# Optimization experiments

Hardware: AMD Instinct MI355X
Metric: run time of the kernel (lower is better)

## Reference

```python
import jax, jax.numpy as jnp
import numpy as np

B, IN, V, H, OUT = 4096, 1024, 48, 512, 64

def setup_inputs() -> dict:
    key = jax.random.key(0)
    ks = jax.random.split(key, 6)
    s = 0.02
    x = jax.random.normal(ks[0], (B, IN), dtype=jnp.float32)
    # stacked per-vocab MLP params: hidden layers have bias, last layer bias=False
    W1 = jax.random.normal(ks[1], (V, IN, H), dtype=jnp.float32) * s
    b1 = jax.random.normal(ks[2], (V, H), dtype=jnp.float32) * s
    W2 = jax.random.normal(ks[3], (V, H, H), dtype=jnp.float32) * s
    b2 = jax.random.normal(ks[4], (V, H), dtype=jnp.float32) * s
    W3 = jax.random.normal(ks[5], (V, H, OUT), dtype=jnp.float32) * s
    return {"x": x, "W1": W1, "b1": b1, "W2": W2, "b2": b2, "W3": W3}

def reference(x, W1, b1, W2, b2, W3):
    # grouped GEMM over the vocab axis; equivalent to the per-MLP loop + cat
    h = jax.nn.relu(jnp.einsum('bi,vih->bvh', x, W1) + b1)      # [B, V, H]
    h = jax.nn.relu(jnp.einsum('bvh,vhk->bvk', h, W2) + b2)     # [B, V, H]
    o = jnp.einsum('bvk,vko->bvo', h, W3)                        # [B, V, OUT]
    # torch.cat([...], dim=-1) == reshape since outputs are in vocab order
    return o.reshape(x.shape[0], V * OUT)
```

## Files before the change

kernel.cpp:

```cpp
#include <hip/hip_runtime.h>

#define B_SZ   4096
#define IN_SZ  1024
#define V_SZ   48
#define H_SZ   512
#define OUT_SZ 64

typedef __attribute__((ext_vector_type(4))) float f32x4;
typedef __attribute__((ext_vector_type(8))) short bf16x8;
typedef __attribute__((ext_vector_type(4))) short short4v;
typedef __attribute__((ext_vector_type(4))) float float4v;

__device__ __forceinline__ short f2bf(float f){
    unsigned u = __builtin_bit_cast(unsigned, f);
    u += 0x7fffu + ((u >> 16) & 1u);
    return (short)(u >> 16);
}

__device__ __forceinline__ void gl2lds16(const void* g, void* l){
    __builtin_amdgcn_global_load_lds(
        (const __attribute__((address_space(1))) void*)g,
        (__attribute__((address_space(3))) void*)l, 16, 0, 0);
}

__global__ void k_convert_x(const float* __restrict__ x, short* __restrict__ xb){
    int i = blockIdx.x * 256 + threadIdx.x;
    float4v f = ((const float4v*)x)[i];
    short4v o = { f2bf(f.x), f2bf(f.y), f2bf(f.z), f2bf(f.w) };
    ((short4v*)xb)[i] = o;
}

__global__ void k_transpose_cvt(const float* __restrict__ in, short* __restrict__ out,
                                int R, int C){
    __shared__ short t[64][66];
    int v  = blockIdx.z;
    int c0 = blockIdx.x * 64, r0 = blockIdx.y * 64;
    int tx = threadIdx.x, ty = threadIdx.y;
    size_t base = (size_t)v * R * C;
    const float* inp = in + base + (size_t)r0 * C + c0;
    #pragma unroll
    for (int j = 0; j < 16; ++j){
        int r = ty + j*4;
        t[r][tx] = f2bf(inp[(size_t)r * C + tx]);
    }
    __syncthreads();
    short* outp = out + base + (size_t)c0 * R + r0;
    #pragma unroll
    for (int j = 0; j < 16; ++j){
        int cc = ty + j*4;
        outp[(size_t)cc * R + tx] = t[tx][cc];
    }
}

__global__ __launch_bounds__(256) void k_gemm1(
    const short* __restrict__ xb, const short* __restrict__ W1t,
    const float* __restrict__ b1, short* __restrict__ h1)
{
    __shared__ __align__(16) short As[128*64];
    __shared__ __align__(16) short Bs[128*64];
    const int tid  = threadIdx.x;
    const int lane = tid & 63, wave = tid >> 6;
    const int l15  = lane & 15, quad = lane >> 4;
    const int wm = wave & 1, wn = wave >> 1;
    const int M0 = blockIdx.x * 128;
    const int N0 = blockIdx.y * 128;
    const int v  = blockIdx.z;

    const short* a_base = xb  + (size_t)M0 * IN_SZ;
    const short* b_base = W1t + ((size_t)v * H_SZ + N0) * IN_SZ;

    const short* asrc[4]; const short* bsrc[4]; short* adst[4]; short* bdst[4];
    #pragma unroll
    for (int j = 0; j < 4; ++j){
        int p   = j*256 + tid;
        int row = p >> 3;
        int w   = (p & 7) ^ (row & 7);
        asrc[j] = a_base + (size_t)row * IN_SZ + w*8;
        bsrc[j] = b_base + (size_t)row * IN_SZ + w*8;
        adst[j] = &As[(size_t)(j*256 + (tid & ~63)) * 8];
        bdst[j] = &Bs[(size_t)(j*256 + (tid & ~63)) * 8];
    }

    f32x4 acc[4][4];
    #pragma unroll
    for (int i = 0; i < 4; ++i)
        #pragma unroll
        for (int j = 0; j < 4; ++j) acc[i][j] = (f32x4){0.f,0.f,0.f,0.f};

    for (int k0 = 0; k0 < IN_SZ; k0 += 64){
        #pragma unroll
        for (int j = 0; j < 4; ++j){
            gl2lds16(asrc[j] + k0, adst[j]);
            gl2lds16(bsrc[j] + k0, bdst[j]);
        }
        __syncthreads();
        #pragma unroll
        for (int kk = 0; kk < 2; ++kk){
            bf16x8 a[4], b[4];
            #pragma unroll
            for (int tm = 0; tm < 4; ++tm){
                int m = wm*64 + tm*16 + l15;
                int slot = m*8 + ((kk*4 + quad) ^ (m & 7));
                a[tm] = *(const bf16x8*)&As[slot*8];
            }
            #pragma unroll
            for (int tn = 0; tn < 4; ++tn){
                int n = wn*64 + tn*16 + l15;
                int slot = n*8 + ((kk*4 + quad) ^ (n & 7));
                b[tn] = *(const bf16x8*)&Bs[slot*8];
            }
            #pragma unroll
            for (int tm = 0; tm < 4; ++tm)
                #pragma unroll
                for (int tn = 0; tn < 4; ++tn)
                    acc[tm][tn] = __builtin_amdgcn_mfma_f32_16x16x32_bf16(
                        a[tm], b[tn], acc[tm][tn], 0, 0, 0);
        }
        __syncthreads();
    }

    const float* b1v = b1 + v * H_SZ;
    short* h1v = h1 + (size_t)v * B_SZ * H_SZ;
    #pragma unroll
    for (int tn = 0; tn < 4; ++tn){
        int col = N0 + wn*64 + tn*16 + l15;
        float bias = b1v[col];
        #pragma unroll
        for (int tm = 0; tm < 4; ++tm){
            int rowb = M0 + wm*64 + tm*16 + quad*4;
            #pragma unroll
            for (int r = 0; r < 4; ++r){
                float val = acc[tm][tn][r] + bias;
                val = val > 0.f ? val : 0.f;
                h1v[(size_t)(rowb + r) * H_SZ + col] = f2bf(val);
            }
        }
    }
}

__global__ __launch_bounds__(512) void k_gemm23(
    const short* __restrict__ h1, const short* __restrict__ W2t,
    const float* __restrict__ b2, const short* __restrict__ W3t,
    float* __restrict__ out)
{
    __shared__ __align__(16) short h2s[128*512];
    __shared__ __align__(16) short As[128*32];
    __shared__ __align__(16) short Bs[256*32];
    const int tid  = threadIdx.x;
    const int lane = tid & 63, wave = tid >> 6;
    const int l15  = lane & 15, quad = lane >> 4;
    const int M0 = blockIdx.x * 128;
    const int v  = blockIdx.y;
    const short* h1v = h1  + (size_t)v * B_SZ * H_SZ + (size_t)M0 * H_SZ;
    const short* w2v = W2t + (size_t)v * H_SZ * H_SZ;
    const float* b2v = b2  + v * H_SZ;
    const short* w3v = W3t + (size_t)v * OUT_SZ * H_SZ;

    const int wm = wave & 1, wn = wave >> 1;

    int pA = tid;
    int wrapA = pA >> 3, posA = (pA & 7) ^ (wrapA & 7);
    int rowA = wrapA*2 + (posA >> 2), wA = posA & 3;
    const short* asrc = h1v + (size_t)rowA * H_SZ + wA*8;
    short* adst = &As[(size_t)(tid & ~63) * 8];
    const short* bsrc[2]; short* bdst[2]; int browg[2];
    #pragma unroll
    for (int j = 0; j < 2; ++j){
        int p = j*512 + tid;
        int wrapI = p >> 3, posL = (p & 7) ^ (wrapI & 7);
        int row = wrapI*2 + (posL >> 2), w = posL & 3;
        browg[j] = row;
        bsrc[j] = w2v + (size_t)row * H_SZ + w*8;
        bdst[j] = &Bs[(size_t)(j*512 + (tid & ~63)) * 8];
    }

    for (int np = 0; np < 2; ++np){
        const int N0 = np * 256;
        f32x4 acc[4][4];
        #pragma unroll
        for (int i = 0; i < 4; ++i)
            #pragma unroll
            for (int j = 0; j < 4; ++j) acc[i][j] = (f32x4){0.f,0.f,0.f,0.f};

        for (int k0 = 0; k0 < H_SZ; k0 += 32){
            gl2lds16(asrc + k0, adst);
            #pragma unroll
            for (int j = 0; j < 2; ++j)
                gl2lds16(bsrc[j] + (size_t)N0 * H_SZ + k0, bdst[j]);
            __syncthreads();
            bf16x8 a[4], b[4];
            #pragma unroll
            for (int tm = 0; tm < 4; ++tm){
                int m = wm*64 + tm*16 + l15;
                int slot = (m>>1)*8 + ((((m&1)<<2) | quad) ^ ((m>>1) & 7));
                a[tm] = *(const bf16x8*)&As[slot*8];
            }
            #pragma unroll
            for (int tn = 0; tn < 4; ++tn){
                int n = wn*64 + tn*16 + l15;
                int slot = (n>>1)*8 + ((((n&1)<<2) | quad) ^ ((n>>1) & 7));
                b[tn] = *(const bf16x8*)&Bs[slot*8];
            }
            #pragma unroll
            for (int tm = 0; tm < 4; ++tm)
                #pragma unroll
                for (int tn = 0; tn < 4; ++tn)
                    acc[tm][tn] = __builtin_amdgcn_mfma_f32_16x16x32_bf16(
                        a[tm], b[tn], acc[tm][tn], 0, 0, 0);
            __syncthreads();
        }
        #pragma unroll
        for (int tn = 0; tn < 4; ++tn){
            int n = N0 + wn*64 + tn*16 + l15;
            float bias = b2v[n];
            int u = n >> 3;
            #pragma unroll
            for (int tm = 0; tm < 4; ++tm){
                int rowb = wm*64 + tm*16 + quad*4;
                #pragma unroll
                for (int r = 0; r < 4; ++r){
                    int row = rowb + r;
                    float val = acc[tm][tn][r] + bias;
                    val = val > 0.f ? val : 0.f;
                    int slot = row*64 + (u ^ (row & 7));
                    h2s[slot*8 + (n & 7)] = f2bf(val);
                }
            }
        }
    }
    __syncthreads();

    const int wn3 = wave & 3, wm3 = wave >> 2;
    f32x4 acc3[4];
    #pragma unroll
    for (int i = 0; i < 4; ++i) acc3[i] = (f32x4){0.f,0.f,0.f,0.f};
    const int n3 = wn3*16 + l15;
    for (int kk = 0; kk < 16; ++kk){
        int kbase = kk*32 + quad*8;
        bf16x8 bfrag = *(const bf16x8*)&w3v[(size_t)n3 * H_SZ + kbase];
        int u = kbase >> 3;
        #pragma unroll
        for (int tm = 0; tm < 4; ++tm){
            int m = wm3*64 + tm*16 + l15;
            int slot = m*64 + (u ^ (m & 7));
            bf16x8 afrag = *(const bf16x8*)&h2s[slot*8];
            acc3[tm] = __builtin_amdgcn_mfma_f32_16x16x32_bf16(afrag, bfrag, acc3[tm], 0, 0, 0);
        }
    }
    #pragma unroll
    for (int tm = 0; tm < 4; ++tm){
        int rowb = M0 + wm3*64 + tm*16 + quad*4;
        int col  = v*OUT_SZ + wn3*16 + l15;
        #pragma unroll
        for (int r = 0; r < 4; ++r)
            out[(size_t)(rowb + r) * (V_SZ*OUT_SZ) + col] = acc3[tm][r];
    }
}

extern "C" void kernel_launch(void* const* d_in, const int* in_sizes, int n_in,
                              void* d_out, int out_size, void* d_ws, size_t ws_size,
                              hipStream_t stream)
{
    (void)in_sizes; (void)n_in; (void)out_size; (void)ws_size;
    const float* x  = (const float*)d_in[0];
    const float* W1 = (const float*)d_in[1];
    const float* b1 = (const float*)d_in[2];
    const float* W2 = (const float*)d_in[3];
    const float* b2 = (const float*)d_in[4];
    const float* W3 = (const float*)d_in[5];
    float* out = (float*)d_out;

    char* ws = (char*)d_ws;
    short* xb  = (short*)ws;  ws += (size_t)B_SZ * IN_SZ * 2;
    short* W1t = (short*)ws;  ws += (size_t)V_SZ * H_SZ * IN_SZ * 2;
    short* W2t = (short*)ws;  ws += (size_t)V_SZ * H_SZ * H_SZ * 2;
    short* W3t = (short*)ws;  ws += (size_t)V_SZ * OUT_SZ * H_SZ * 2;
    short* h1  = (short*)ws;

    k_convert_x<<<dim3(B_SZ*IN_SZ/1024), dim3(256), 0, stream>>>(x, xb);
    k_transpose_cvt<<<dim3(H_SZ/64,  IN_SZ/64, V_SZ), dim3(64,4), 0, stream>>>(W1, W1t, IN_SZ, H_SZ);
    k_transpose_cvt<<<dim3(H_SZ/64,  H_SZ/64,  V_SZ), dim3(64,4), 0, stream>>>(W2, W2t, H_SZ, H_SZ);
    k_transpose_cvt<<<dim3(OUT_SZ/64,H_SZ/64,  V_SZ), dim3(64,4), 0, stream>>>(W3, W3t, H_SZ, OUT_SZ);
    k_gemm1 <<<dim3(B_SZ/128, H_SZ/128, V_SZ), dim3(256), 0, stream>>>(xb, W1t, b1, h1);
    k_gemm23<<<dim3(B_SZ/128, V_SZ),           dim3(512), 0, stream>>>(h1, W2t, b2, W3t, out);
}
```

Before: 717.7 us.

## Split fused GEMM2+GEMM3 kernel into in-place GEMM2 and separate GEMM3

Replaces the fused layer-2/layer-3 kernel, which kept a 128x512 h2 tile in LDS, with two kernels. The first computes layer 2 for a 64-row block across all 512 columns with BK=64 and writes the bf16 result back over h1 in place. The second reads h2 from global memory and does the 64-wide output GEMM with 128x64 tiles. This cuts LDS use per block and drops the N-pass loop, aiming for higher occupancy and fewer barriers, at the cost of an extra global round-trip of h2 and one more launch.

After: 723.0 us. No clear change (+0.7%).

```diff
diff --git a/kernel.cpp b/kernel.cpp
--- a/kernel.cpp
+++ b/kernel.cpp
@@ -119,86 +119,79 @@
         __syncthreads();
     }
 
-    const float* b1v = b1 + v * H_SZ;
-    short* h1v = h1 + (size_t)v * B_SZ * H_SZ;
+    const float* bv = b1 + (size_t)v * H_SZ;
+    short* cv = h1 + (size_t)v * (B_SZ*H_SZ);
     #pragma unroll
     for (int tn = 0; tn < 4; ++tn){
         int col = N0 + wn*64 + tn*16 + l15;
-        float bias = b1v[col];
+        float bb = bv[col];
         #pragma unroll
         for (int tm = 0; tm < 4; ++tm){
             int rowb = M0 + wm*64 + tm*16 + quad*4;
             #pragma unroll
             for (int r = 0; r < 4; ++r){
-                float val = acc[tm][tn][r] + bias;
+                float val = acc[tm][tn][r] + bb;
                 val = val > 0.f ? val : 0.f;
-                h1v[(size_t)(rowb + r) * H_SZ + col] = f2bf(val);
-            }
-        }
-    }
-}
-
-__global__ __launch_bounds__(512) void k_gemm23(
-    const short* __restrict__ h1, const short* __restrict__ W2t,
-    const float* __restrict__ b2, const short* __restrict__ W3t,
-    float* __restrict__ out)
+                cv[(size_t)(rowb + r) * H_SZ + col] = f2bf(val);
+            }
+        }
+    }
+}
+
+__global__ __launch_bounds__(512) void k_gemm2_inplace(
+    short* __restrict__ h, const short* __restrict__ W2t,
+    const float* __restrict__ b2)
 {
-    __shared__ __align__(16) short h2s[128*512];
-    __shared__ __align__(16) short As[128*32];
-    __shared__ __align__(16) short Bs[256*32];
+    __shared__ __align__(16) short As[64*64];
+    __shared__ __align__(16) short Bs[512*64];
     const int tid  = threadIdx.x;
     const int lane = tid & 63, wave = tid >> 6;
     const int l15  = lane & 15, quad = lane >> 4;
-    const int M0 = blockIdx.x * 128;
+    const int M0 = blockIdx.x * 64;
     const int v  = blockIdx.y;
-    const short* h1v = h1  + (size_t)v * B_SZ * H_SZ + (size_t)M0 * H_SZ;
-    const short* w2v = W2t + (size_t)v * H_SZ * H_SZ;
-    const float* b2v = b2  + v * H_SZ;
-    const short* w3v = W3t + (size_t)v * OUT_SZ * H_SZ;
-
-    const int wm = wave & 1, wn = wave >> 1;
-
-    int pA = tid;
-    int wrapA = pA >> 3, posA = (pA & 7) ^ (wrapA & 7);
-    int rowA = wrapA*2 + (posA >> 2), wA = posA & 3;
-    const short* asrc = h1v + (size_t)rowA * H_SZ + wA*8;
+
+    short* hv = h + (size_t)v * (B_SZ*H_SZ) + (size_t)M0 * H_SZ;
+    const short* w2v = W2t + (size_t)v * (H_SZ*H_SZ);
+
+    int rowA = tid >> 3;
+    int wA   = (tid & 7) ^ (rowA & 7);
+    const short* asrc = hv + (size_t)rowA * H_SZ + wA*8;
     short* adst = &As[(size_t)(tid & ~63) * 8];
-    const short* bsrc[2]; short* bdst[2]; int browg[2];
-    #pragma unroll
-    for (int j = 0; j < 2; ++j){
-        int p = j*512 + tid;
-        int wrapI = p >> 3, posL = (p & 7) ^ (wrapI & 7);
-        int row = wrapI*2 + (posL >> 2), w = posL & 3;
-        browg[j] = row;
+    const short* bsrc[8]; short* bdst[8];
+    #pragma unroll
+    for (int j = 0; j < 8; ++j){
+        int p   = j*512 + tid;
+        int row = p >> 3;
+        int w   = (p & 7) ^ (row & 7);
         bsrc[j] = w2v + (size_t)row * H_SZ + w*8;
         bdst[j] = &Bs[(size_t)(j*512 + (tid & ~63)) * 8];
     }
 
-    for (int np = 0; np < 2; ++np){
-        const int N0 = np * 256;
-        f32x4 acc[4][4];
-        #pragma unroll
-        for (int i = 0; i < 4; ++i)
-            #pragma unroll
-            for (int j = 0; j < 4; ++j) acc[i][j] = (f32x4){0.f,0.f,0.f,0.f};
-
-        for (int k0 = 0; k0 < H_SZ; k0 += 32){
-            gl2lds16(asrc + k0, adst);
-            #pragma unroll
-            for (int j = 0; j < 2; ++j)
-                gl2lds16(bsrc[j] + (size_t)N0 * H_SZ + k0, bdst[j]);
-            __syncthreads();
+    f32x4 acc[4][4];
+    #pragma unroll
+    for (int i = 0; i < 4; ++i)
+        #pragma unroll
+        for (int j = 0; j < 4; ++j) acc[i][j] = (f32x4){0.f,0.f,0.f,0.f};
+
+    for (int k0 = 0; k0 < H_SZ; k0 += 64){
+        gl2lds16(asrc + k0, adst);
+        #pragma unroll
+        for (int j = 0; j < 8; ++j)
+            gl2lds16(bsrc[j] + k0, bdst[j]);
+        __syncthreads();
+        #pragma unroll
+        for (int kk = 0; kk < 2; ++kk){
             bf16x8 a[4], b[4];
             #pragma unroll
             for (int tm = 0; tm < 4; ++tm){
-                int m = wm*64 + tm*16 + l15;
-                int slot = (m>>1)*8 + ((((m&1)<<2) | quad) ^ ((m>>1) & 7));
+                int m = tm*16 + l15;
+                int slot = m*8 + ((kk*4 + quad) ^ (m & 7));
                 a[tm] = *(const bf16x8*)&As[slot*8];
             }
             #pragma unroll
             for (int tn = 0; tn < 4; ++tn){
-                int n = wn*64 + tn*16 + l15;
-                int slot = (n>>1)*8 + ((((n&1)<<2) | quad) ^ ((n>>1) & 7));
+                int n = wave*64 + tn*16 + l15;
+                int slot = n*8 + ((kk*4 + quad) ^ (n & 7));
                 b[tn] = *(const bf16x8*)&Bs[slot*8];
             }
             #pragma unroll
@@ -207,53 +200,110 @@
                 for (int tn = 0; tn < 4; ++tn)
                     acc[tm][tn] = __builtin_amdgcn_mfma_f32_16x16x32_bf16(
                         a[tm], b[tn], acc[tm][tn], 0, 0, 0);
-            __syncthreads();
-        }
-        #pragma unroll
-        for (int tn = 0; tn < 4; ++tn){
-            int n = N0 + wn*64 + tn*16 + l15;
-            float bias = b2v[n];
-            int u = n >> 3;
+        }
+        __syncthreads();
+    }
+
+    const float* bv = b2 + (size_t)v * H_SZ;
+    #pragma unroll
+    for (int tn = 0; tn < 4; ++tn){
+        int col = wave*64 + tn*16 + l15;
+        float bb = bv[col];
+        #pragma unroll
+        for (int tm = 0; tm < 4; ++tm){
+            int rowb = tm*16 + quad*4;
+            #pragma unroll
+            for (int r = 0; r < 4; ++r){
+                float val = acc[tm][tn][r] + bb;
+                val = val > 0.f ? val : 0.f;
+                hv[(size_t)(rowb + r) * H_SZ + col] = f2bf(val);
+            }
+        }
+    }
+}
+
+__global__ __launch_bounds__(256) void k_gemm3(
+    const short* __restrict__ h2, const short* __restrict__ W3t,
+    float* __restrict__ out)
+{
+    __shared__ __align__(16) short As[128*64];
+    __shared__ __align__(16) short Bs[64*64];
+    const int tid  = threadIdx.x;
+    const int lane = tid & 63, wave = tid >> 6;
+    const int l15  = lane & 15, quad = lane >> 4;
+    const int wm = wave & 1, wn = wave >> 1;
+    const int M0 = blockIdx.x * 128;
+    const int v  = blockIdx.y;
+
+    const short* a_base = h2  + (size_t)v * (B_SZ*H_SZ) + (size_t)M0 * H_SZ;
+    const short* b_base = W3t + (size_t)v * (OUT_SZ*H_SZ);
+
+    const short* asrc[4]; short* adst[4];
+    #pragma unroll
+    for (int j = 0; j < 4; ++j){
+        int p = j*256 + tid;
+        int row = p >> 3;
+        int w   = (p & 7) ^ (row & 7);
+        asrc[j] = a_base + (size_t)row * H_SZ + w*8;
+        adst[j] = &As[(size_t)(j*256 + (tid & ~63)) * 8];
+    }
+    const short* bsrc[2]; short* bdst[2];
+    #pragma unroll
+    for (int j = 0; j < 2; ++j){
+        int p = j*256 + tid;
+        int row = p >> 3;
+        int w   = (p & 7) ^ (row & 7);
+        bsrc[j] = b_base + (size_t)row * H_SZ + w*8;
+        bdst[j] = &Bs[(size_t)(j*256 + (tid & ~63)) * 8];
+    }
+
+    f32x4 acc[4][2];
+    #pragma unroll
+    for (int i = 0; i < 4; ++i)
+        #pragma unroll
+        for (int j = 0; j < 2; ++j) acc[i][j] = (f32x4){0.f,0.f,0.f,0.f};
+
+    for (int k0 = 0; k0 < H_SZ; k0 += 64){
+        #pragma unroll
+        for (int j = 0; j < 4; ++j) gl2lds16(asrc[j] + k0, adst[j]);
+        #pragma unroll
+        for (int j = 0; j < 2; ++j) gl2lds16(bsrc[j] + k0, bdst[j]);
+        __syncthreads();
+        #pragma unroll
+        for (int kk = 0; kk < 2; ++kk){
+            bf16x8 a[4], b[2];
             #pragma unroll
             for (int tm = 0; tm < 4; ++tm){
-                int rowb = wm*64 + tm*16 + quad*4;
+                int m = wm*64 + tm*16 + l15;
+                int slot = m*8 + ((kk*4 + quad) ^ (m & 7));
+                a[tm] = *(const bf16x8*)&As[slot*8];
+            }
+            #pragma unroll
+            for (int tn = 0; tn < 2; ++tn){
+                int n = wn*32 + tn*16 + l15;
+                int slot = n*8 + ((kk*4 + quad) ^ (n & 7));
+                b[tn] = *(const bf16x8*)&Bs[slot*8];
+            }
+            #pragma unroll
+            for (int tm = 0; tm < 4; ++tm)
                 #pragma unroll
-                for (int r = 0; r < 4; ++r){
-                    int row = rowb + r;
-                    float val = acc[tm][tn][r] + bias;
-                    val = val > 0.f ? val : 0.f;
-                    int slot = row*64 + (u ^ (row & 7));
-                    h2s[slot*8 + (n & 7)] = f2bf(val);
-                }
-            }
-        }
-    }
-    __syncthreads();
-
-    const int wn3 = wave & 3, wm3 = wave >> 2;
-    f32x4 acc3[4];
-    #pragma unroll
-    for (int i = 0; i < 4; ++i) acc3[i] = (f32x4){0.f,0.f,0.f,0.f};
-    const int n3 = wn3*16 + l15;
-    for (int kk = 0; kk < 16; ++kk){
-        int kbase = kk*32 + quad*8;
-        bf16x8 bfrag = *(const bf16x8*)&w3v[(size_t)n3 * H_SZ + kbase];
-        int u = kbase >> 3;
+                for (int tn = 0; tn < 2; ++tn)
+                    acc[tm][tn] = __builtin_amdgcn_mfma_f32_16x16x32_bf16(
+                        a[tm], b[tn], acc[tm][tn], 0, 0, 0);
+        }
+        __syncthreads();
+    }
+
+    #pragma unroll
+    for (int tn = 0; tn < 2; ++tn){
+        int col = v*OUT_SZ + wn*32 + tn*16 + l15;
         #pragma unroll
         for (int tm = 0; tm < 4; ++tm){
-            int m = wm3*64 + tm*16 + l15;
-            int slot = m*64 + (u ^ (m & 7));
-            bf16x8 afrag = *(const bf16x8*)&h2s[slot*8];
-            acc3[tm] = __builtin_amdgcn_mfma_f32_16x16x32_bf16(afrag, bfrag, acc3[tm], 0, 0, 0);
-        }
-    }
-    #pragma unroll
-    for (int tm = 0; tm < 4; ++tm){
-        int rowb = M0 + wm3*64 + tm*16 + quad*4;
-        int col  = v*OUT_SZ + wn3*16 + l15;
-        #pragma unroll
-        for (int r = 0; r < 4; ++r)
-            out[(size_t)(rowb + r) * (V_SZ*OUT_SZ) + col] = acc3[tm][r];
+            int rowb = M0 + wm*64 + tm*16 + quad*4;
+            #pragma unroll
+            for (int r = 0; r < 4; ++r)
+                out[(size_t)(rowb + r) * (V_SZ*OUT_SZ) + col] = acc[tm][tn][r];
+        }
     }
 }
 
@@ -281,6 +331,8 @@
     k_transpose_cvt<<<dim3(H_SZ/64,  IN_SZ/64, V_SZ), dim3(64,4), 0, stream>>>(W1, W1t, IN_SZ, H_SZ);
     k_transpose_cvt<<<dim3(H_SZ/64,  H_SZ/64,  V_SZ), dim3(64,4), 0, stream>>>(W2, W2t, H_SZ, H_SZ);
     k_transpose_cvt<<<dim3(OUT_SZ/64,H_SZ/64,  V_SZ), dim3(64,4), 0, stream>>>(W3, W3t, H_SZ, OUT_SZ);
-    k_gemm1 <<<dim3(B_SZ/128, H_SZ/128, V_SZ), dim3(256), 0, stream>>>(xb, W1t, b1, h1);
-    k_gemm23<<<dim3(B_SZ/128, V_SZ),           dim3(512), 0, stream>>>(h1, W2t, b2, W3t, out);
-}
+
+    k_gemm1<<<dim3(B_SZ/128, H_SZ/128, V_SZ), dim3(256), 0, stream>>>(xb, W1t, b1, h1);
+    k_gemm2_inplace<<<dim3(B_SZ/64, V_SZ), dim3(512), 0, stream>>>(h1, W2t, b2);
+    k_gemm3<<<dim3(B_SZ/128, V_SZ), dim3(256), 0, stream>>>(h1, W3t, out);
+}
```

## Retile fused GEMM2/3 to 64-row blocks over full N and vectorize weight transposes

Applied to the files above, without the earlier changes.

The fused second and third GEMM now uses 64-row M tiles with each block covering all 512 hidden columns in one pass, using a K step of 64 and reusing the B staging buffer to hold the hidden activations for the final projection. This removes the two-pass N loop and the separate 128KB h2 buffer. LDS use drops and grid size doubles, but W2 is reloaded by twice as many blocks, and only half the waves take part in the last GEMM. The weight transpose/convert kernel is also rewritten to use float4 loads and short4 stores with 256-thread 1D blocks.

Result: faster. 653.9 us (-8.9%).

```diff
diff --git a/kernel.cpp b/kernel.cpp
--- a/kernel.cpp
+++ b/kernel.cpp
@@ -30,25 +30,32 @@
     ((short4v*)xb)[i] = o;
 }
 
-__global__ void k_transpose_cvt(const float* __restrict__ in, short* __restrict__ out,
-                                int R, int C){
-    __shared__ short t[64][66];
+__global__ __launch_bounds__(256) void k_transpose_cvt4(
+    const float* __restrict__ in, short* __restrict__ out, int R, int C)
+{
+    __shared__ short t[64][68];
     int v  = blockIdx.z;
     int c0 = blockIdx.x * 64, r0 = blockIdx.y * 64;
-    int tx = threadIdx.x, ty = threadIdx.y;
+    int tid = threadIdx.x;
     size_t base = (size_t)v * R * C;
     const float* inp = in + base + (size_t)r0 * C + c0;
-    #pragma unroll
-    for (int j = 0; j < 16; ++j){
-        int r = ty + j*4;
-        t[r][tx] = f2bf(inp[(size_t)r * C + tx]);
+    int g    = tid >> 4;
+    int col4 = (tid & 15) * 4;
+    #pragma unroll
+    for (int p = 0; p < 4; ++p){
+        int row = p*16 + g;
+        float4v f = *(const float4v*)&inp[(size_t)row * C + col4];
+        short4v s = { f2bf(f.x), f2bf(f.y), f2bf(f.z), f2bf(f.w) };
+        *(short4v*)&t[row][col4] = s;
     }
     __syncthreads();
     short* outp = out + base + (size_t)c0 * R + r0;
-    #pragma unroll
-    for (int j = 0; j < 16; ++j){
-        int cc = ty + j*4;
-        outp[(size_t)cc * R + tx] = t[tx][cc];
+    int r4 = (tid & 15) * 4;
+    #pragma unroll
+    for (int p = 0; p < 4; ++p){
+        int c = p*16 + g;
+        short4v s = { t[r4+0][c], t[r4+1][c], t[r4+2][c], t[r4+3][c] };
+        *(short4v*)&outp[(size_t)c * R + r4] = s;
     }
 }
 
@@ -119,86 +126,74 @@
         __syncthreads();
     }
 
-    const float* b1v = b1 + v * H_SZ;
-    short* h1v = h1 + (size_t)v * B_SZ * H_SZ;
+    const float* bv = b1 + (size_t)v * H_SZ;
+    short* cv = h1 + (size_t)v * (B_SZ*H_SZ);
     #pragma unroll
     for (int tn = 0; tn < 4; ++tn){
         int col = N0 + wn*64 + tn*16 + l15;
-        float bias = b1v[col];
+        float bb = bv[col];
         #pragma unroll
         for (int tm = 0; tm < 4; ++tm){
             int rowb = M0 + wm*64 + tm*16 + quad*4;
             #pragma unroll
             for (int r = 0; r < 4; ++r){
-                float val = acc[tm][tn][r] + bias;
+                float val = acc[tm][tn][r] + bb;
                 val = val > 0.f ? val : 0.f;
-                h1v[(size_t)(rowb + r) * H_SZ + col] = f2bf(val);
+                cv[(size_t)(rowb + r) * H_SZ + col] = f2bf(val);
             }
         }
     }
 }
 
 __global__ __launch_bounds__(512) void k_gemm23(
-    const short* __restrict__ h1, const short* __restrict__ W2t,
+    const short* __restrict__ h, const short* __restrict__ W2t,
     const float* __restrict__ b2, const short* __restrict__ W3t,
     float* __restrict__ out)
 {
-    __shared__ __align__(16) short h2s[128*512];
-    __shared__ __align__(16) short As[128*32];
-    __shared__ __align__(16) short Bs[256*32];
+    __shared__ __align__(16) short As[64*64];
+    __shared__ __align__(16) short Bs[512*64];
     const int tid  = threadIdx.x;
     const int lane = tid & 63, wave = tid >> 6;
     const int l15  = lane & 15, quad = lane >> 4;
-    const int M0 = blockIdx.x * 128;
+    const int M0 = blockIdx.x * 64;
     const int v  = blockIdx.y;
-    const short* h1v = h1  + (size_t)v * B_SZ * H_SZ + (size_t)M0 * H_SZ;
-    const short* w2v = W2t + (size_t)v * H_SZ * H_SZ;
-    const float* b2v = b2  + v * H_SZ;
-    const short* w3v = W3t + (size_t)v * OUT_SZ * H_SZ;
-
-    const int wm = wave & 1, wn = wave >> 1;
-
-    int pA = tid;
-    int wrapA = pA >> 3, posA = (pA & 7) ^ (wrapA & 7);
-    int rowA = wrapA*2 + (posA >> 2), wA = posA & 3;
-    const short* asrc = h1v + (size_t)rowA * H_SZ + wA*8;
-    short* adst = &As[(size_t)(tid & ~63) * 8];
-    const short* bsrc[2]; short* bdst[2]; int browg[2];
-    #pragma unroll
-    for (int j = 0; j < 2; ++j){
-        int p = j*512 + tid;
-        int wrapI = p >> 3, posL = (p & 7) ^ (wrapI & 7);
-        int row = wrapI*2 + (posL >> 2), w = posL & 3;
-        browg[j] = row;
-        bsrc[j] = w2v + (size_t)row * H_SZ + w*8;
-        bdst[j] = &Bs[(size_t)(j*512 + (tid & ~63)) * 8];
-    }
-
-    for (int np = 0; np < 2; ++np){
-        const int N0 = np * 256;
-        f32x4 acc[4][4];
-        #pragma unroll
-        for (int i = 0; i < 4; ++i)
-            #pragma unroll
-            for (int j = 0; j < 4; ++j) acc[i][j] = (f32x4){0.f,0.f,0.f,0.f};
-
-        for (int k0 = 0; k0 < H_SZ; k0 += 32){
-            gl2lds16(asrc + k0, adst);
-            #pragma unroll
-            for (int j = 0; j < 2; ++j)
-                gl2lds16(bsrc[j] + (size_t)N0 * H_SZ + k0, bdst[j]);
-            __syncthreads();
+
+    const short* hv  = h   + (size_t)v * (B_SZ*H_SZ) + (size_t)M0 * H_SZ;
+    const short* w2v = W2t + (size_t)v * (H_SZ*H_SZ);
+    const short* w3v = W3t + (size_t)v * (OUT_SZ*H_SZ);
+
+    const int rowT = tid >> 3;
+    const int wT   = (tid & 7) ^ (rowT & 7);
+    const short* asrc  = hv  + (size_t)rowT * H_SZ + wT*8;
+    const short* bsrc0 = w2v + (size_t)rowT * H_SZ + wT*8;
+    short* adst  = &As[(size_t)(tid & ~63) * 8];
+    short* bdst0 = &Bs[(size_t)(tid & ~63) * 8];
+
+    f32x4 acc[4][4];
+    #pragma unroll
+    for (int i = 0; i < 4; ++i)
+        #pragma unroll
+        for (int j = 0; j < 4; ++j) acc[i][j] = (f32x4){0.f,0.f,0.f,0.f};
+
+    for (int k0 = 0; k0 < H_SZ; k0 += 64){
+        gl2lds16(asrc + k0, adst);
+        #pragma unroll
+        for (int j = 0; j < 8; ++j)
+            gl2lds16(bsrc0 + (size_t)j*(64*H_SZ) + k0, bdst0 + (size_t)j*512*8);
+        __syncthreads();
+        #pragma unroll
+        for (int kk = 0; kk < 2; ++kk){
             bf16x8 a[4], b[4];
             #pragma unroll
             for (int tm = 0; tm < 4; ++tm){
-                int m = wm*64 + tm*16 + l15;
-                int slot = (m>>1)*8 + ((((m&1)<<2) | quad) ^ ((m>>1) & 7));
+                int m = tm*16 + l15;
+                int slot = m*8 + ((kk*4 + quad) ^ (m & 7));
                 a[tm] = *(const bf16x8*)&As[slot*8];
             }
             #pragma unroll
             for (int tn = 0; tn < 4; ++tn){
-                int n = wn*64 + tn*16 + l15;
-                int slot = (n>>1)*8 + ((((n&1)<<2) | quad) ^ ((n>>1) & 7));
+                int n = wave*64 + tn*16 + l15;
+                int slot = n*8 + ((kk*4 + quad) ^ (n & 7));
                 b[tn] = *(const bf16x8*)&Bs[slot*8];
             }
             #pragma unroll
@@ -207,53 +202,56 @@
                 for (int tn = 0; tn < 4; ++tn)
                     acc[tm][tn] = __builtin_amdgcn_mfma_f32_16x16x32_bf16(
                         a[tm], b[tn], acc[tm][tn], 0, 0, 0);
-            __syncthreads();
-        }
-        #pragma unroll
-        for (int tn = 0; tn < 4; ++tn){
-            int n = N0 + wn*64 + tn*16 + l15;
-            float bias = b2v[n];
-            int u = n >> 3;
+        }
+        __syncthreads();
+    }
+
+    const float* bv = b2 + (size_t)v * H_SZ;
+    #pragma unroll
+    for (int tn = 0; tn < 4; ++tn){
+        int col = wave*64 + tn*16 + l15;
+        float bb = bv[col];
+        int u = col >> 3, c7 = col & 7;
+        #pragma unroll
+        for (int tm = 0; tm < 4; ++tm){
+            int rowb = tm*16 + quad*4;
+            #pragma unroll
+            for (int r = 0; r < 4; ++r){
+                int row = rowb + r;
+                float val = acc[tm][tn][r] + bb;
+                val = val > 0.f ? val : 0.f;
+                Bs[row*512 + ((u ^ (row & 7))*8) + c7] = f2bf(val);
+            }
+        }
+    }
+    __syncthreads();
+
+    if (wave < 4){
+        f32x4 acc3[4];
+        #pragma unroll
+        for (int i = 0; i < 4; ++i) acc3[i] = (f32x4){0.f,0.f,0.f,0.f};
+        const int n3 = wave*16 + l15;
+        const short* b3p = &w3v[(size_t)n3 * H_SZ + quad*8];
+        #pragma unroll
+        for (int kk = 0; kk < 16; ++kk){
+            bf16x8 bfrag = *(const bf16x8*)&b3p[kk*32];
+            int u = kk*4 + quad;
             #pragma unroll
             for (int tm = 0; tm < 4; ++tm){
-                int rowb = wm*64 + tm*16 + quad*4;
-                #pragma unroll
-                for (int r = 0; r < 4; ++r){
-                    int row = rowb + r;
-                    float val = acc[tm][tn][r] + bias;
-                    val = val > 0.f ? val : 0.f;
-                    int slot = row*64 + (u ^ (row & 7));
-                    h2s[slot*8 + (n & 7)] = f2bf(val);
-                }
-            }
-        }
-    }
-    __syncthreads();
-
-    const int wn3 = wave & 3, wm3 = wave >> 2;
-    f32x4 acc3[4];
-    #pragma unroll
-    for (int i = 0; i < 4; ++i) acc3[i] = (f32x4){0.f,0.f,0.f,0.f};
-    const int n3 = wn3*16 + l15;
-    for (int kk = 0; kk < 16; ++kk){
-        int kbase = kk*32 + quad*8;
-        bf16x8 bfrag = *(const bf16x8*)&w3v[(size_t)n3 * H_SZ + kbase];
-        int u = kbase >> 3;
+                int m = tm*16 + l15;
+                bf16x8 afrag = *(const bf16x8*)&Bs[m*512 + ((u ^ (m & 7))*8)];
+                acc3[tm] = __builtin_amdgcn_mfma_f32_16x16x32_bf16(
+                    afrag, bfrag, acc3[tm], 0, 0, 0);
+            }
+        }
+        const int col = v*OUT_SZ + wave*16 + l15;
         #pragma unroll
         for (int tm = 0; tm < 4; ++tm){
-            int m = wm3*64 + tm*16 + l15;
-            int slot = m*64 + (u ^ (m & 7));
-            bf16x8 afrag = *(const bf16x8*)&h2s[slot*8];
-            acc3[tm] = __builtin_amdgcn_mfma_f32_16x16x32_bf16(afrag, bfrag, acc3[tm], 0, 0, 0);
-        }
-    }
-    #pragma unroll
-    for (int tm = 0; tm < 4; ++tm){
-        int rowb = M0 + wm3*64 + tm*16 + quad*4;
-        int col  = v*OUT_SZ + wn3*16 + l15;
-        #pragma unroll
-        for (int r = 0; r < 4; ++r)
-            out[(size_t)(rowb + r) * (V_SZ*OUT_SZ) + col] = acc3[tm][r];
+            int rowb = M0 + tm*16 + quad*4;
+            #pragma unroll
+            for (int r = 0; r < 4; ++r)
+                out[(size_t)(rowb + r) * (V_SZ*OUT_SZ) + col] = acc3[tm][r];
+        }
     }
 }
 
@@ -278,9 +276,10 @@
     short* h1  = (short*)ws;
 
     k_convert_x<<<dim3(B_SZ*IN_SZ/1024), dim3(256), 0, stream>>>(x, xb);
-    k_transpose_cvt<<<dim3(H_SZ/64,  IN_SZ/64, V_SZ), dim3(64,4), 0, stream>>>(W1, W1t, IN_SZ, H_SZ);
-    k_transpose_cvt<<<dim3(H_SZ/64,  H_SZ/64,  V_SZ), dim3(64,4), 0, stream>>>(W2, W2t, H_SZ, H_SZ);
-    k_transpose_cvt<<<dim3(OUT_SZ/64,H_SZ/64,  V_SZ), dim3(64,4), 0, stream>>>(W3, W3t, H_SZ, OUT_SZ);
+    k_transpose_cvt4<<<dim3(H_SZ/64,  IN_SZ/64, V_SZ), dim3(256), 0, stream>>>(W1, W1t, IN_SZ, H_SZ);
+    k_transpose_cvt4<<<dim3(H_SZ/64,  H_SZ/64,  V_SZ), dim3(256), 0, stream>>>(W2, W2t, H_SZ, H_SZ);
+    k_transpose_cvt4<<<dim3(OUT_SZ/64,H_SZ/64,  V_SZ), dim3(256), 0, stream>>>(W3, W3t, H_SZ, OUT_SZ);
+
     k_gemm1 <<<dim3(B_SZ/128, H_SZ/128, V_SZ), dim3(256), 0, stream>>>(xb, W1t, b1, h1);
-    k_gemm23<<<dim3(B_SZ/128, V_SZ),           dim3(512), 0, stream>>>(h1, W2t, b2, W3t, out);
-}
+    k_gemm23<<<dim3(B_SZ/64, V_SZ), dim3(512), 0, stream>>>(h1, W2t, b2, W3t, out);
+}
```
